# Kernel optimization log

Hardware: AMD Instinct MI355X
Metric: run time of the kernel (lower is better)

The kernel has to match this reference:

```python
import jax, jax.numpy as jnp
import numpy as np

V = 8192        # variants
NREF = 262144   # total ref reads
NALT = 131072   # total alt reads
F_READ = 11     # tensors.NUM_READ_FEATURES
F_INFO = 9      # tensors.NUM_INFO_FEATURES
H = 256         # hidden width
MAX_ALT = 10


def setup_inputs() -> dict:
    key = jax.random.key(0)
    ks = jax.random.split(key, 24)
    p = lambda k, shp: (jax.random.normal(k, shp, dtype=jnp.float32) * 0.05)
    inp = {
        "reads": jax.random.normal(ks[0], (NREF + NALT, F_READ), dtype=jnp.float32),
        "info": jax.random.normal(ks[1], (V, F_INFO), dtype=jnp.float32),
        "ref_seg_ids": jnp.sort(jax.random.randint(ks[2], (NREF,), 0, V, dtype=jnp.int32)),
        "alt_seg_ids": jnp.sort(jax.random.randint(ks[3], (NALT,), 0, V, dtype=jnp.int32)),
        "variant_types": jax.random.randint(ks[4], (V,), 0, 3, dtype=jnp.int32),
        # phi: [F_READ, H, H]
        "phi_W0": p(ks[5], (F_READ, H)), "phi_b0": p(ks[6], (H,)),
        "phi_W1": p(ks[7], (H, H)), "phi_b1": p(ks[8], (H,)),
        # omega: [F_INFO, H]
        "om_W0": p(ks[9], (F_INFO, H)), "om_b0": p(ks[10], (H,)),
        # rho: [3H, H, H]
        "rho_W0": p(ks[11], (3 * H, H)), "rho_b0": p(ks[12], (H,)),
        "rho_W1": p(ks[13], (H, H)), "rho_b1": p(ks[14], (H,)),
        # 3 output MLPs, stacked: [H,H] -> [H,1]
        "out_W1": p(ks[15], (3, H, H)), "out_b1": p(ks[16], (3, H)),
        "out_W2": p(ks[17], (3, H, 1)), "out_b2": p(ks[18], (3, 1)),
        # calibration
        "conf": jnp.sqrt(jnp.arange(0, MAX_ALT + 1, dtype=jnp.float32)),
        "max_logit": jnp.array(10.0, dtype=jnp.float32),
    }
    return inp


def _seg_mean(x, seg_ids, num_segments):
    sums = jax.ops.segment_sum(x, seg_ids, num_segments=num_segments)
    counts = jax.ops.segment_sum(jnp.ones((x.shape[0],), x.dtype), seg_ids, num_segments=num_segments)
    return sums / jnp.maximum(counts, 1.0)[:, None], counts


def reference(reads, info, ref_seg_ids, alt_seg_ids, variant_types,
              phi_W0, phi_b0, phi_W1, phi_b1, om_W0, om_b0,
              rho_W0, rho_b0, rho_W1, rho_b1,
              out_W1, out_b1, out_W2, out_b2, conf, max_logit):
    lrelu = jax.nn.leaky_relu
    # phi MLP (leaky_relu between layers, none after last), then sigmoid
    h = lrelu(reads @ phi_W0 + phi_b0)
    phi_reads = jax.nn.sigmoid(h @ phi_W1 + phi_b1)          # [N, H]
    ref_reads = phi_reads[:NREF]
    alt_reads = phi_reads[NREF:]
    ref_means, _ = _seg_mean(ref_reads, ref_seg_ids, V)       # [V, H]
    alt_means, alt_counts = _seg_mean(alt_reads, alt_seg_ids, V)
    omega_info = jax.nn.sigmoid(info @ om_W0 + om_b0)         # [V, H]
    concat = jnp.concatenate([ref_means, alt_means, omega_info], axis=1)  # [V, 3H]
    agg = lrelu(concat @ rho_W0 + rho_b0) @ rho_W1 + rho_b1   # [V, H]
    # per-variant-type output MLPs, select by variant type
    o = lrelu(jnp.einsum('vd,tde->tve', agg, out_W1) + out_b1[:, None, :])
    outs = (jnp.einsum('tve,teo->tvo', o, out_W2) + out_b2[:, None, :])[:, :, 0]  # [3, V]
    logits = jnp.take_along_axis(outs, variant_types[None, :].astype(jnp.int32), axis=0)[0]
    # calibration
    trunc = jnp.minimum(alt_counts.astype(jnp.int32), MAX_ALT)
    logits = logits * conf[trunc]
    return max_logit * jnp.tanh(logits / max_logit)
```

## Files before the change

kernel.cpp:

```cpp
#include <hip/hip_runtime.h>
#include <hip/hip_bf16.h>
#include <cmath>

#define V 8192
#define NREF 262144
#define NALT 131072
#define NREADS (NREF + NALT)
#define FR 11
#define FI 9
#define HH 256
#define MAX_ALT 10

#define TILE_R 128
#define TILE_V 32

#define HPITCH 264
#define RBPITCH 40
#define CPITCH 776
#define APITCH 264

typedef short bf16x8 __attribute__((ext_vector_type(8)));
typedef float f32x4  __attribute__((ext_vector_type(4)));

__device__ __forceinline__ float sigmoidf_(float x) {
    return __builtin_amdgcn_rcpf(1.0f + __expf(-x));
}
__device__ __forceinline__ float lrelu_(float x) {
    return x > 0.0f ? x : 0.01f * x;
}
__device__ __forceinline__ unsigned short f2bf_(float f) {
    unsigned int u = __float_as_uint(f);
    u += 0x7FFFu + ((u >> 16) & 1u);
    return (unsigned short)(u >> 16);
}
__device__ __forceinline__ float bf2f_(unsigned short b) {
    return __uint_as_float(((unsigned int)b) << 16);
}
__device__ __forceinline__ unsigned int pk2bf_(float a, float b) {
    union { __hip_bfloat162 h2; unsigned int u; } cvt;
    cvt.h2 = __float22bfloat162_rn(make_float2(a, b));
    return cvt.u;
}

__global__ __launch_bounds__(256) void prep_kernel(
    const float* __restrict__ phi_W1, const float* __restrict__ rho_W0,
    const float* __restrict__ rho_W1, const float* __restrict__ out_W1,
    const float* __restrict__ phi_W0,
    unsigned short* __restrict__ w1t_phi, unsigned short* __restrict__ w0t,
    unsigned short* __restrict__ w1rt, unsigned short* __restrict__ whT,
    unsigned short* __restrict__ w0pT)
{
    __shared__ unsigned short sT[32][33];
    const int b = blockIdx.x;
    const int t = threadIdx.x;
    if (b < 512) {
        const float* src; unsigned short* dst; int R, C, bx, by;
        if (b < 64)       { src = phi_W1; dst = w1t_phi; R = 256; C = 256; bx = b & 7; by = b >> 3; }
        else if (b < 256) { int i = b - 64;  src = rho_W0; dst = w0t;  R = 768; C = 256; bx = i & 7; by = i >> 3; }
        else if (b < 320) { int i = b - 256; src = rho_W1; dst = w1rt; R = 256; C = 256; bx = i & 7; by = i >> 3; }
        else              { int i = b - 320; int z = i >> 6; i &= 63;
                            src = out_W1 + (size_t)z * HH * HH; dst = whT + (size_t)z * HH * HH;
                            R = 256; C = 256; bx = i & 7; by = i >> 3; }
        const int tx = t & 31, ty = t >> 5;
        const int r0 = by * 32, c0 = bx * 32;
#pragma unroll
        for (int k = 0; k < 4; k++)
            sT[ty + k * 8][tx] = f2bf_(src[(size_t)(r0 + ty + k * 8) * C + c0 + tx]);
        __syncthreads();
#pragma unroll
        for (int k = 0; k < 4; k++)
            dst[(size_t)(c0 + ty + k * 8) * R + r0 + tx] = sT[tx][ty + k * 8];
    } else {
        const int idx = (b - 512) * 256 + t;
        const int c = idx >> 5, k = idx & 31;
        unsigned short v = 0;
        if (k < FR) v = f2bf_(phi_W0[k * HH + c]);
        else if (k >= 16 && k < 16 + FR) v = f2bf_(phi_W0[(k - 16) * HH + c]);
        w0pT[idx] = v;
    }
}

__global__ __launch_bounds__(512, 2) void phi_seg_kernel(
    const float* __restrict__ reads,
    const int* __restrict__ ref_ids, const int* __restrict__ alt_ids,
    const unsigned short* __restrict__ w0pT, const float* __restrict__ b0,
    const unsigned short* __restrict__ w1t, const float* __restrict__ b1,
    float* __restrict__ ref_sums, float* __restrict__ alt_sums,
    int* __restrict__ ref_cnt, int* __restrict__ alt_cnt)
{
    __shared__ __align__(16) unsigned short sH[TILE_R * HPITCH];
    __shared__ __align__(16) unsigned short sRB[TILE_R * RBPITCH];

    const int t  = threadIdx.x;
    const int r0 = blockIdx.x * TILE_R;
    const bool is_ref = (r0 < NREF);
    const int* seg_ids = is_ref ? ref_ids : alt_ids;
    const int sbase    = is_ref ? r0 : (r0 - NREF);
    float* sums = is_ref ? ref_sums : alt_sums;
    int*   cnts = is_ref ? ref_cnt  : alt_cnt;

    {
        const int row = t & 127, q = t >> 7;
        const float* rp = reads + (size_t)(r0 + row) * FR;
        const int nj = (q & 1) ? 3 : 8;
        const int cb = (q & 1) ? 8 : 0;
        unsigned short o[8];
#pragma unroll
        for (int j = 0; j < 8; j++) o[j] = 0;
        if (q < 2) {
            for (int j = 0; j < nj; j++) o[j] = f2bf_(rp[cb + j]);
        } else {
            for (int j = 0; j < nj; j++) {
                float f = rp[cb + j];
                o[j] = f2bf_(f - bf2f_(f2bf_(f)));
            }
        }
        uint4 pk;
        pk.x = (unsigned int)o[0] | ((unsigned int)o[1] << 16);
        pk.y = (unsigned int)o[2] | ((unsigned int)o[3] << 16);
        pk.z = (unsigned int)o[4] | ((unsigned int)o[5] << 16);
        pk.w = (unsigned int)o[6] | ((unsigned int)o[7] << 16);
        *(uint4*)&sRB[row * RBPITCH + q * 8] = pk;
    }
    __syncthreads();

    const int wv   = t >> 6;
    const int lane = t & 63;
    const int lrow = lane & 15;
    const int quad = lane >> 4;

    {
        bf16x8 br[8];
#pragma unroll
        for (int rt = 0; rt < 8; rt++)
            br[rt] = *(const bf16x8*)&sRB[(rt * 16 + lrow) * RBPITCH + quad * 8];

#pragma unroll
        for (int cm = 0; cm < 2; cm++) {
            const bf16x8 aw = *(const bf16x8*)(w0pT + ((wv * 32 + cm * 16 + lrow) << 5) + quad * 8);
            f32x4 c1[8];
#pragma unroll
            for (int rt = 0; rt < 8; rt++)
                c1[rt] = __builtin_amdgcn_mfma_f32_16x16x32_bf16(
                    aw, br[rt], (f32x4){0.f, 0.f, 0.f, 0.f}, 0, 0, 0);

            const float4 bias = *(const float4*)(b0 + wv * 32 + cm * 16 + quad * 4);
#pragma unroll
            for (int rt = 0; rt < 8; rt++) {
                const int r = rt * 16 + lrow;
                uint2 pk;
                pk.x = pk2bf_(lrelu_(c1[rt][0] + bias.x), lrelu_(c1[rt][1] + bias.y));
                pk.y = pk2bf_(lrelu_(c1[rt][2] + bias.z), lrelu_(c1[rt][3] + bias.w));
                *(uint2*)&sH[r * HPITCH + wv * 32 + cm * 16 + quad * 4] = pk;
            }
        }
    }
    __syncthreads();

    f32x4 acc[8][2];
#pragma unroll
    for (int mt = 0; mt < 8; mt++)
#pragma unroll
        for (int nt = 0; nt < 2; nt++)
            acc[mt][nt] = (f32x4){0.f, 0.f, 0.f, 0.f};

#pragma unroll
    for (int kk = 0; kk < 8; kk++) {
        const bf16x8 bn0 = *(const bf16x8*)(w1t + (size_t)(wv * 32 + lrow) * HH + kk * 32 + quad * 8);
        const bf16x8 bn1 = *(const bf16x8*)(w1t + (size_t)(wv * 32 + 16 + lrow) * HH + kk * 32 + quad * 8);
#pragma unroll
        for (int mt = 0; mt < 8; mt++) {
            const bf16x8 am = *(const bf16x8*)&sH[(mt * 16 + lrow) * HPITCH + kk * 32 + quad * 8];
            acc[mt][0] = __builtin_amdgcn_mfma_f32_16x16x32_bf16(am, bn0, acc[mt][0], 0, 0, 0);
            acc[mt][1] = __builtin_amdgcn_mfma_f32_16x16x32_bf16(am, bn1, acc[mt][1], 0, 0, 0);
        }
    }

#pragma unroll
    for (int nt = 0; nt < 2; nt++) {
        const float bb = b1[wv * 32 + nt * 16 + lrow];
#pragma unroll
        for (int mt = 0; mt < 8; mt++)
#pragma unroll
            for (int r = 0; r < 4; r++)
                acc[mt][nt][r] = sigmoidf_(acc[mt][nt][r] + bb);
    }

#pragma unroll
    for (int g = 0; g < 2; g++) {
        const int myseg = seg_ids[sbase + g * 64 + lane];
        const int prev  = __shfl_up(myseg, 1);
        const bool flag = (lane == 0) || (myseg != prev);
        unsigned long long m = __ballot(flag);

        while (m) {
            const int start = (int)__builtin_ctzll(m);
            const unsigned long long m2 = m & (m - 1);
            const int end = m2 ? (int)__builtin_ctzll(m2) : 64;
            m = m2;
            const int seg = __shfl(myseg, start);
            float* srow = sums + (size_t)seg * HH + wv * 32;

            float msk[4][4];
#pragma unroll
            for (int lm = 0; lm < 4; lm++)
#pragma unroll
                for (int r = 0; r < 4; r++) {
                    const int lrw = lm * 16 + quad * 4 + r;
                    msk[lm][r] = (lrw >= start && lrw < end) ? 1.0f : 0.0f;
                }
#pragma unroll
            for (int nt = 0; nt < 2; nt++) {
                float s = 0.f;
#pragma unroll
                for (int lm = 0; lm < 4; lm++)
#pragma unroll
                    for (int r = 0; r < 4; r++)
                        s = fmaf(acc[g * 4 + lm][nt][r], msk[lm][r], s);
                s += __shfl_down(s, 32);
                s += __shfl_down(s, 16);
                if (quad == 0)
                    atomicAdd(&srow[nt * 16 + lrow], s);
            }
            if (t == 0) atomicAdd(&cnts[seg], end - start);
        }
    }
}

__global__ __launch_bounds__(1024, 1) void rho_mfma_kernel(
    const float* __restrict__ info, const int* __restrict__ vtypes,
    const float* __restrict__ om_W0, const float* __restrict__ om_b0,
    const unsigned short* __restrict__ w0t, const float* __restrict__ rho_b0,
    const unsigned short* __restrict__ w1rt, const float* __restrict__ rho_b1,
    const unsigned short* __restrict__ whT, const float* __restrict__ out_b1,
    const float* __restrict__ out_W2, const float* __restrict__ out_b2,
    const float* __restrict__ conf, const float* __restrict__ max_logit,
    const float* __restrict__ ref_sums, const float* __restrict__ alt_sums,
    const int* __restrict__ ref_cnt, const int* __restrict__ alt_cnt,
    float* __restrict__ out)
{
    __shared__ __align__(16) unsigned short sC[TILE_V * CPITCH];
    __shared__ __align__(16) float sInfo[TILE_V][12];
    __shared__ float sRinvR[TILE_V], sRinvA[TILE_V];
    __shared__ float sPart[16][3][TILE_V];

    unsigned short* sA1  = sC;
    unsigned short* sAgg = sC + TILE_V * APITCH;

    const int t  = threadIdx.x;
    const int v0 = blockIdx.x * TILE_V;

    if (t < TILE_V) {
        sRinvR[t] = __builtin_amdgcn_rcpf(fmaxf((float)ref_cnt[v0 + t], 1.0f));
        sRinvA[t] = __builtin_amdgcn_rcpf(fmaxf((float)alt_cnt[v0 + t], 1.0f));
    }
    for (int idx = t; idx < TILE_V * FI; idx += 1024) {
        int i = idx / FI, k = idx - i * FI;
        sInfo[i][k] = info[(size_t)(v0 + i) * FI + k];
    }
    __syncthreads();

    {
        const int c = t & 255, grp = t >> 8;
        float om0r[FI];
#pragma unroll
        for (int k = 0; k < FI; k++) om0r[k] = om_W0[k * HH + c];
        const float omb = om_b0[c];
#pragma unroll
        for (int ii = 0; ii < 8; ii++) {
            const int i = grp * 8 + ii, v = v0 + i;
            float rm = ref_sums[(size_t)v * HH + c] * sRinvR[i];
            float am = alt_sums[(size_t)v * HH + c] * sRinvA[i];
            float a = omb;
#pragma unroll
            for (int k = 0; k < FI; k++) a = fmaf(sInfo[i][k], om0r[k], a);
            sC[i * CPITCH + c]          = f2bf_(rm);
            sC[i * CPITCH + HH + c]     = f2bf_(am);
            sC[i * CPITCH + 2 * HH + c] = f2bf_(sigmoidf_(a));
        }
    }
    __syncthreads();

    const int wv   = t >> 6;
    const int lane = t & 63;
    const int lrow = lane & 15;
    const int quad = lane >> 4;
    const int ncol = wv * 16 + lrow;

    f32x4 p1[2] = {(f32x4){0.f,0.f,0.f,0.f}, (f32x4){0.f,0.f,0.f,0.f}};
#pragma unroll 4
    for (int kk = 0; kk < 24; kk++) {
        bf16x8 a0 = *(const bf16x8*)&sC[lrow * CPITCH + kk * 32 + quad * 8];
        bf16x8 a1 = *(const bf16x8*)&sC[(16 + lrow) * CPITCH + kk * 32 + quad * 8];
        bf16x8 bn = *(const bf16x8*)(w0t + (size_t)ncol * 768 + kk * 32 + quad * 8);
        p1[0] = __builtin_amdgcn_mfma_f32_16x16x32_bf16(a0, bn, p1[0], 0, 0, 0);
        p1[1] = __builtin_amdgcn_mfma_f32_16x16x32_bf16(a1, bn, p1[1], 0, 0, 0);
    }
    __syncthreads();
    {
        const float bb = rho_b0[ncol];
#pragma unroll
        for (int mt = 0; mt < 2; mt++)
#pragma unroll
            for (int r = 0; r < 4; r++) {
                const int row = mt * 16 + quad * 4 + r;
                sA1[row * APITCH + ncol] = f2bf_(lrelu_(p1[mt][r] + bb));
            }
    }
    __syncthreads();

    f32x4 p2[2] = {(f32x4){0.f,0.f,0.f,0.f}, (f32x4){0.f,0.f,0.f,0.f}};
#pragma unroll
    for (int kk = 0; kk < 8; kk++) {
        bf16x8 a0 = *(const bf16x8*)&sA1[lrow * APITCH + kk * 32 + quad * 8];
        bf16x8 a1 = *(const bf16x8*)&sA1[(16 + lrow) * APITCH + kk * 32 + quad * 8];
        bf16x8 bn = *(const bf16x8*)(w1rt + (size_t)ncol * HH + kk * 32 + quad * 8);
        p2[0] = __builtin_amdgcn_mfma_f32_16x16x32_bf16(a0, bn, p2[0], 0, 0, 0);
        p2[1] = __builtin_amdgcn_mfma_f32_16x16x32_bf16(a1, bn, p2[1], 0, 0, 0);
    }
    {
        const float bb = rho_b1[ncol];
#pragma unroll
        for (int mt = 0; mt < 2; mt++)
#pragma unroll
            for (int r = 0; r < 4; r++) {
                const int row = mt * 16 + quad * 4 + r;
                sAgg[row * APITCH + ncol] = f2bf_(p2[mt][r] + bb);
            }
    }
    __syncthreads();

    bf16x8 aF[8][2];
#pragma unroll
    for (int kk = 0; kk < 8; kk++)
#pragma unroll
        for (int mt = 0; mt < 2; mt++)
            aF[kk][mt] = *(const bf16x8*)&sAgg[(mt * 16 + lrow) * APITCH + kk * 32 + quad * 8];

    for (int h = 0; h < 3; h++) {
        f32x4 p3[2] = {(f32x4){0.f,0.f,0.f,0.f}, (f32x4){0.f,0.f,0.f,0.f}};
#pragma unroll
        for (int kk = 0; kk < 8; kk++) {
            bf16x8 bn = *(const bf16x8*)(whT + ((size_t)h * HH + ncol) * HH + kk * 32 + quad * 8);
            p3[0] = __builtin_amdgcn_mfma_f32_16x16x32_bf16(aF[kk][0], bn, p3[0], 0, 0, 0);
            p3[1] = __builtin_amdgcn_mfma_f32_16x16x32_bf16(aF[kk][1], bn, p3[1], 0, 0, 0);
        }
        const float bb = out_b1[h * HH + ncol];
        const float w2 = out_W2[h * HH + ncol];
#pragma unroll
        for (int mt = 0; mt < 2; mt++)
#pragma unroll
            for (int r = 0; r < 4; r++) {
                float v = lrelu_(p3[mt][r] + bb) * w2;
                v += __shfl_down(v, 8);
                v += __shfl_down(v, 4);
                v += __shfl_down(v, 2);
                v += __shfl_down(v, 1);
                if (lrow == 0) sPart[wv][h][mt * 16 + quad * 4 + r] = v;
            }
    }
    __syncthreads();

    if (t < TILE_V) {
        const int v = v0 + t;
        const int ty = vtypes[v];
        float logit = 0.f;
#pragma unroll
        for (int w = 0; w < 16; w++) logit += sPart[w][ty][t];
        logit += out_b2[ty];
        const int tr = min(alt_cnt[v], MAX_ALT);
        logit *= conf[tr];
        const float ml = max_logit[0];
        out[v] = ml * tanhf(logit / ml);
    }
}

extern "C" void kernel_launch(void* const* d_in, const int* in_sizes, int n_in,
                              void* d_out, int out_size, void* d_ws, size_t ws_size,
                              hipStream_t stream) {
    const float* reads    = (const float*)d_in[0];
    const float* info     = (const float*)d_in[1];
    const int*   ref_ids  = (const int*)d_in[2];
    const int*   alt_ids  = (const int*)d_in[3];
    const int*   vtypes   = (const int*)d_in[4];
    const float* phi_W0   = (const float*)d_in[5];
    const float* phi_b0   = (const float*)d_in[6];
    const float* phi_W1   = (const float*)d_in[7];
    const float* phi_b1   = (const float*)d_in[8];
    const float* om_W0    = (const float*)d_in[9];
    const float* om_b0    = (const float*)d_in[10];
    const float* rho_W0   = (const float*)d_in[11];
    const float* rho_b0   = (const float*)d_in[12];
    const float* rho_W1   = (const float*)d_in[13];
    const float* rho_b1   = (const float*)d_in[14];
    const float* out_W1   = (const float*)d_in[15];
    const float* out_b1   = (const float*)d_in[16];
    const float* out_W2   = (const float*)d_in[17];
    const float* out_b2   = (const float*)d_in[18];
    const float* conf     = (const float*)d_in[19];
    const float* max_lg   = (const float*)d_in[20];
    float* out = (float*)d_out;

    float* ref_sums = (float*)d_ws;
    float* alt_sums = ref_sums + (size_t)V * HH;
    int*   ref_cnt  = (int*)(alt_sums + (size_t)V * HH);
    int*   alt_cnt  = ref_cnt + V;
    unsigned short* w1t_phi = (unsigned short*)(alt_cnt + V);
    unsigned short* w0t     = w1t_phi + (size_t)HH * HH;
    unsigned short* w1rt    = w0t + (size_t)HH * 768;
    unsigned short* whT     = w1rt + (size_t)HH * HH;
    unsigned short* w0pT    = whT + (size_t)3 * HH * HH;

    const size_t zero_bytes = (size_t)2 * V * HH * sizeof(float) + (size_t)2 * V * sizeof(int);
    hipMemsetAsync(d_ws, 0, zero_bytes, stream);

    prep_kernel<<<544, 256, 0, stream>>>(phi_W1, rho_W0, rho_W1, out_W1, phi_W0,
                                         w1t_phi, w0t, w1rt, whT, w0pT);

    phi_seg_kernel<<<NREADS / TILE_R, 512, 0, stream>>>(
        reads, ref_ids, alt_ids, w0pT, phi_b0, w1t_phi, phi_b1,
        ref_sums, alt_sums, ref_cnt, alt_cnt);

    rho_mfma_kernel<<<V / TILE_V, 1024, 0, stream>>>(
        info, vtypes, om_W0, om_b0, w0t, rho_b0, w1rt, rho_b1,
        whT, out_b1, out_W2, out_b2, conf, max_lg,
        ref_sums, alt_sums, ref_cnt, alt_cnt, out);
}
```

Before: 249.9 us.

## Reduce segment sums through shared-memory slab before global atomics

The per-wave ballot/shuffle segment loop is replaced by LDS atomics into a shared slab indexed by segment offset within the tile, which is then flushed to global sums with one atomic per segment column. Counts become one atomic per row, and read loading is made branch-free with hi/lo bf16 split. The aim is fewer global atomics and less divergent loop work, at the cost of LDS atomic contention, extra syncs and slab zeroing. The rho kernel is also launched a second time, which adds redundant work.

Result: slower. 750.1 us (+200.1%).

```diff
diff --git a/kernel.cpp b/kernel.cpp
--- a/kernel.cpp
+++ b/kernel.cpp
@@ -18,6 +18,9 @@
 #define RBPITCH 40
 #define CPITCH 776
 #define APITCH 264
+
+#define SLOTCAP 64
+#define SLABP   66
 
 typedef short bf16x8 __attribute__((ext_vector_type(8)));
 typedef float f32x4  __attribute__((ext_vector_type(4)));
@@ -90,6 +93,7 @@
 {
     __shared__ __align__(16) unsigned short sH[TILE_R * HPITCH];
     __shared__ __align__(16) unsigned short sRB[TILE_R * RBPITCH];
+    __shared__ __align__(16) int sSegL[TILE_R];
 
     const int t  = threadIdx.x;
     const int r0 = blockIdx.x * TILE_R;
@@ -102,18 +106,18 @@
     {
         const int row = t & 127, q = t >> 7;
         const float* rp = reads + (size_t)(r0 + row) * FR;
-        const int nj = (q & 1) ? 3 : 8;
+        const bool hiSel = (q < 2);
         const int cb = (q & 1) ? 8 : 0;
         unsigned short o[8];
 #pragma unroll
-        for (int j = 0; j < 8; j++) o[j] = 0;
-        if (q < 2) {
-            for (int j = 0; j < nj; j++) o[j] = f2bf_(rp[cb + j]);
-        } else {
-            for (int j = 0; j < nj; j++) {
-                float f = rp[cb + j];
-                o[j] = f2bf_(f - bf2f_(f2bf_(f)));
-            }
+        for (int j = 0; j < 8; j++) {
+            const int f = cb + j;
+            const int fc = (f < FR) ? f : (FR - 1);
+            float x = rp[fc];
+            x = (f < FR) ? x : 0.f;
+            const unsigned short hi = f2bf_(x);
+            const unsigned short lo = f2bf_(x - bf2f_(hi));
+            o[j] = hiSel ? hi : lo;
         }
         uint4 pk;
         pk.x = (unsigned int)o[0] | ((unsigned int)o[1] << 16);
@@ -122,6 +126,7 @@
         pk.w = (unsigned int)o[6] | ((unsigned int)o[7] << 16);
         *(uint4*)&sRB[row * RBPITCH + q * 8] = pk;
     }
+    if (t < TILE_R) sSegL[t] = seg_ids[sbase + t];
     __syncthreads();
 
     const int wv   = t >> 6;
@@ -186,43 +191,67 @@
                 acc[mt][nt][r] = sigmoidf_(acc[mt][nt][r] + bb);
     }
 
-#pragma unroll
-    for (int g = 0; g < 2; g++) {
-        const int myseg = seg_ids[sbase + g * 64 + lane];
-        const int prev  = __shfl_up(myseg, 1);
-        const bool flag = (lane == 0) || (myseg != prev);
-        unsigned long long m = __ballot(flag);
-
-        while (m) {
-            const int start = (int)__builtin_ctzll(m);
-            const unsigned long long m2 = m & (m - 1);
-            const int end = m2 ? (int)__builtin_ctzll(m2) : 64;
-            m = m2;
-            const int seg = __shfl(myseg, start);
-            float* srow = sums + (size_t)seg * HH + wv * 32;
-
-            float msk[4][4];
-#pragma unroll
-            for (int lm = 0; lm < 4; lm++)
+    __syncthreads();
+
+    float* slab = (float*)sH;
+
+    {
+        float4 z = {0.f, 0.f, 0.f, 0.f};
+        for (int i = t; i < 256 * SLABP / 4; i += 512) ((float4*)slab)[i] = z;
+    }
+    if (t < TILE_R) atomicAdd(&cnts[sSegL[t]], 1);
+
+    const int s0   = sSegL[0];
+    const int span = sSegL[TILE_R - 1] - s0 + 1;
+
+    __syncthreads();
+
+    const int colb0 = (wv * 32 + lrow) * SLABP;
+    const int colb1 = (wv * 32 + 16 + lrow) * SLABP;
+
+    if (span <= SLOTCAP) {
+#pragma unroll
+        for (int mt = 0; mt < 8; mt++) {
+            const int4 sg = *(const int4*)&sSegL[mt * 16 + quad * 4];
+            const int so_[4] = {sg.x - s0, sg.y - s0, sg.z - s0, sg.w - s0};
+#pragma unroll
+            for (int r = 0; r < 4; r++) {
+                atomicAdd(&slab[colb0 + so_[r]], acc[mt][0][r]);
+                atomicAdd(&slab[colb1 + so_[r]], acc[mt][1][r]);
+            }
+        }
+        __syncthreads();
+        for (int i = t; i < span * 256; i += 512) {
+            const int slot = i >> 8, col = i & 255;
+            atomicAdd(&sums[(size_t)(s0 + slot) * HH + col], slab[col * SLABP + slot]);
+        }
+    } else {
+        for (int base = 0; base < span; base += SLOTCAP) {
+            if (base) {
+                __syncthreads();
+                float4 z = {0.f, 0.f, 0.f, 0.f};
+                for (int i = t; i < 256 * SLABP / 4; i += 512) ((float4*)slab)[i] = z;
+                __syncthreads();
+            }
+#pragma unroll
+            for (int mt = 0; mt < 8; mt++) {
+                const int4 sg = *(const int4*)&sSegL[mt * 16 + quad * 4];
+                const int so_[4] = {sg.x - s0 - base, sg.y - s0 - base,
+                                    sg.z - s0 - base, sg.w - s0 - base};
 #pragma unroll
                 for (int r = 0; r < 4; r++) {
-                    const int lrw = lm * 16 + quad * 4 + r;
-                    msk[lm][r] = (lrw >= start && lrw < end) ? 1.0f : 0.0f;
+                    if (so_[r] >= 0 && so_[r] < SLOTCAP) {
+                        atomicAdd(&slab[colb0 + so_[r]], acc[mt][0][r]);
+                        atomicAdd(&slab[colb1 + so_[r]], acc[mt][1][r]);
+                    }
                 }
-#pragma unroll
-            for (int nt = 0; nt < 2; nt++) {
-                float s = 0.f;
-#pragma unroll
-                for (int lm = 0; lm < 4; lm++)
-#pragma unroll
-                    for (int r = 0; r < 4; r++)
-                        s = fmaf(acc[g * 4 + lm][nt][r], msk[lm][r], s);
-                s += __shfl_down(s, 32);
-                s += __shfl_down(s, 16);
-                if (quad == 0)
-                    atomicAdd(&srow[nt * 16 + lrow], s);
-            }
-            if (t == 0) atomicAdd(&cnts[seg], end - start);
+            }
+            __syncthreads();
+            const int ns = min(span - base, SLOTCAP);
+            for (int i = t; i < ns * 256; i += 512) {
+                const int slot = i >> 8, col = i & 255;
+                atomicAdd(&sums[(size_t)(s0 + base + slot) * HH + col], slab[col * SLABP + slot]);
+            }
         }
     }
 }
@@ -425,4 +454,8 @@
         info, vtypes, om_W0, om_b0, w0t, rho_b0, w1rt, rho_b1,
         whT, out_b1, out_W2, out_b2, conf, max_lg,
         ref_sums, alt_sums, ref_cnt, alt_cnt, out);
-}
+    rho_mfma_kernel<<<V / TILE_V, 1024, 0, stream>>>(
+        info, vtypes, om_W0, om_b0, w0t, rho_b0, w1rt, rho_b1,
+        whT, out_b1, out_W2, out_b2, conf, max_lg,
+        ref_sums, alt_sums, ref_cnt, alt_cnt, out);
+}
```

## Fold workspace zeroing into prep kernel and simplify segment masking and sigmoid

Applied to the files above, without the earlier changes.

Removes the separate hipMemsetAsync by adding extra blocks to prep_kernel that zero the sums and counts workspace with float4 stores. This saves one launch and one stream dependency. The segmented reduction now stages segment ids in shared memory and selects values by comparing each row's id to the current segment, replacing the range-mask construction. The sigmoid is rewritten with exp2 and a pre-scaled bias so it needs one FMA and no separate multiply. The cost is extra blocks in the prep launch and a small shared-memory array.

Result: no change. 248.5 us (-0.6%).

```diff
diff --git a/kernel.cpp b/kernel.cpp
--- a/kernel.cpp
+++ b/kernel.cpp
@@ -22,11 +22,11 @@
 typedef short bf16x8 __attribute__((ext_vector_type(8)));
 typedef float f32x4  __attribute__((ext_vector_type(4)));
 
+__device__ __forceinline__ float lrelu_(float x) {
+    return x > 0.0f ? x : 0.01f * x;
+}
 __device__ __forceinline__ float sigmoidf_(float x) {
     return __builtin_amdgcn_rcpf(1.0f + __expf(-x));
-}
-__device__ __forceinline__ float lrelu_(float x) {
-    return x > 0.0f ? x : 0.01f * x;
 }
 __device__ __forceinline__ unsigned short f2bf_(float f) {
     unsigned int u = __float_as_uint(f);
@@ -48,7 +48,7 @@
     const float* __restrict__ phi_W0,
     unsigned short* __restrict__ w1t_phi, unsigned short* __restrict__ w0t,
     unsigned short* __restrict__ w1rt, unsigned short* __restrict__ whT,
-    unsigned short* __restrict__ w0pT)
+    unsigned short* __restrict__ w0pT, float* __restrict__ zbase)
 {
     __shared__ unsigned short sT[32][33];
     const int b = blockIdx.x;
@@ -70,13 +70,18 @@
 #pragma unroll
         for (int k = 0; k < 4; k++)
             dst[(size_t)(c0 + ty + k * 8) * R + r0 + tx] = sT[tx][ty + k * 8];
-    } else {
+    } else if (b < 544) {
         const int idx = (b - 512) * 256 + t;
         const int c = idx >> 5, k = idx & 31;
         unsigned short v = 0;
         if (k < FR) v = f2bf_(phi_W0[k * HH + c]);
         else if (k >= 16 && k < 16 + FR) v = f2bf_(phi_W0[(k - 16) * HH + c]);
         w0pT[idx] = v;
+    } else {
+        const int n4 = (2 * V * HH + 2 * V) / 4;
+        float4 z = {0.f, 0.f, 0.f, 0.f};
+        for (int i = (b - 544) * 256 + t; i < n4; i += 1024 * 256)
+            ((float4*)zbase)[i] = z;
     }
 }
 
@@ -90,6 +95,7 @@
 {
     __shared__ __align__(16) unsigned short sH[TILE_R * HPITCH];
     __shared__ __align__(16) unsigned short sRB[TILE_R * RBPITCH];
+    __shared__ __align__(16) int sSegL[TILE_R];
 
     const int t  = threadIdx.x;
     const int r0 = blockIdx.x * TILE_R;
@@ -122,6 +128,7 @@
         pk.w = (unsigned int)o[6] | ((unsigned int)o[7] << 16);
         *(uint4*)&sRB[row * RBPITCH + q * 8] = pk;
     }
+    if (t < TILE_R) sSegL[t] = seg_ids[sbase + t];
     __syncthreads();
 
     const int wv   = t >> 6;
@@ -176,14 +183,17 @@
         }
     }
 
+    const float L2E = 1.44269504f;
 #pragma unroll
     for (int nt = 0; nt < 2; nt++) {
-        const float bb = b1[wv * 32 + nt * 16 + lrow];
+        const float nb = -b1[wv * 32 + nt * 16 + lrow] * L2E;
 #pragma unroll
         for (int mt = 0; mt < 8; mt++)
 #pragma unroll
-            for (int r = 0; r < 4; r++)
-                acc[mt][nt][r] = sigmoidf_(acc[mt][nt][r] + bb);
+            for (int r = 0; r < 4; r++) {
+                const float e = __builtin_amdgcn_exp2f(fmaf(acc[mt][nt][r], -L2E, nb));
+                acc[mt][nt][r] = __builtin_amdgcn_rcpf(1.0f + e);
+            }
     }
 
 #pragma unroll
@@ -193,22 +203,20 @@
         const bool flag = (lane == 0) || (myseg != prev);
         unsigned long long m = __ballot(flag);
 
+        int sgl[4][4];
+#pragma unroll
+        for (int lm = 0; lm < 4; lm++) {
+            const int4 s4 = *(const int4*)&sSegL[g * 64 + lm * 16 + quad * 4];
+            sgl[lm][0] = s4.x; sgl[lm][1] = s4.y; sgl[lm][2] = s4.z; sgl[lm][3] = s4.w;
+        }
+
         while (m) {
             const int start = (int)__builtin_ctzll(m);
-            const unsigned long long m2 = m & (m - 1);
-            const int end = m2 ? (int)__builtin_ctzll(m2) : 64;
-            m = m2;
+            m &= m - 1;
+            const int end = m ? (int)__builtin_ctzll(m) : 64;
             const int seg = __shfl(myseg, start);
             float* srow = sums + (size_t)seg * HH + wv * 32;
 
-            float msk[4][4];
-#pragma unroll
-            for (int lm = 0; lm < 4; lm++)
-#pragma unroll
-                for (int r = 0; r < 4; r++) {
-                    const int lrw = lm * 16 + quad * 4 + r;
-                    msk[lm][r] = (lrw >= start && lrw < end) ? 1.0f : 0.0f;
-                }
 #pragma unroll
             for (int nt = 0; nt < 2; nt++) {
                 float s = 0.f;
@@ -216,7 +224,7 @@
                 for (int lm = 0; lm < 4; lm++)
 #pragma unroll
                     for (int r = 0; r < 4; r++)
-                        s = fmaf(acc[g * 4 + lm][nt][r], msk[lm][r], s);
+                        s += (sgl[lm][r] == seg) ? acc[g * 4 + lm][nt][r] : 0.f;
                 s += __shfl_down(s, 32);
                 s += __shfl_down(s, 16);
                 if (quad == 0)
@@ -411,11 +419,9 @@
     unsigned short* whT     = w1rt + (size_t)HH * HH;
     unsigned short* w0pT    = whT + (size_t)3 * HH * HH;
 
-    const size_t zero_bytes = (size_t)2 * V * HH * sizeof(float) + (size_t)2 * V * sizeof(int);
-    hipMemsetAsync(d_ws, 0, zero_bytes, stream);
-
-    prep_kernel<<<544, 256, 0, stream>>>(phi_W1, rho_W0, rho_W1, out_W1, phi_W0,
-                                         w1t_phi, w0t, w1rt, whT, w0pT);
+    prep_kernel<<<1568, 256, 0, stream>>>(phi_W1, rho_W0, rho_W1, out_W1, phi_W0,
+                                          w1t_phi, w0t, w1rt, whT, w0pT,
+                                          (float*)d_ws);
 
     phi_seg_kernel<<<NREADS / TILE_R, 512, 0, stream>>>(
         reads, ref_ids, alt_ids, w0pT, phi_b0, w1t_phi, phi_b1,
```
